# Performance work log

Measured on AMD Instinct MI355X. Metric: run time of the kernel, lower is better.

The kernel has to match this reference:

```python
import jax, jax.numpy as jnp
import numpy as np

PAD = -999
BATCH, NCHAIN, SEQ, NALT, NRES = 8, 2, 1024, 3, 20
NATOMS = 2_000_000
NATNAMES = 40
BACKBONE = jnp.array([0, 1, 2, 3], dtype=jnp.int32)  # N, CA, C, O atom-name ids
GLY = 7  # residue id treated as glycine (rsaSC forced to 0)
NBINS = BATCH * NCHAIN * SEQ * NALT


def setup_inputs() -> dict:
    key = jax.random.key(0)
    k = jax.random.split(key, 8)
    contRat = jax.random.uniform(k[0], (NATOMS, NALT), dtype=jnp.float32)
    atname = jax.random.randint(k[1], (NATOMS,), 0, NATNAMES, dtype=jnp.int32)
    # assign each atom to a (batch, chain, resnum) residue consistently
    resid = jax.random.randint(k[2], (NATOMS,), 0, BATCH * NCHAIN * SEQ, dtype=jnp.int32)
    batch = resid // (NCHAIN * SEQ)
    chain = (resid // SEQ) % NCHAIN
    resnum = resid % SEQ
    # residue type is a function of the residue (consistent across its atoms)
    resname_per_res = jax.random.randint(k[3], (BATCH * NCHAIN * SEQ,), 0, NRES, dtype=jnp.int32)
    resname = resname_per_res[resid]
    atom_description = jnp.stack([atname, resnum, chain, batch, resname], axis=1)
    alternatives = jax.random.bernoulli(k[4], 0.7, (NATOMS, NALT))
    # per-residue-type affine normalization points (max, min), max > min
    resMC_min = jax.random.uniform(k[5], (NRES,), dtype=jnp.float32) * 2.0
    resMC_max = resMC_min + 10.0 + jax.random.uniform(k[6], (NRES,), dtype=jnp.float32) * 20.0
    resSC_min = jax.random.uniform(k[7], (NRES,), dtype=jnp.float32) * 2.0
    resSC_max = resSC_min + 10.0 + jax.random.uniform(jax.random.fold_in(key, 99), (NRES,), dtype=jnp.float32) * 20.0
    return {
        "contRat": contRat,
        "resMC_max": resMC_max,
        "resMC_min": resMC_min,
        "resSC_max": resSC_max,
        "resSC_min": resSC_min,
        "atom_description": atom_description,
        "alternatives": alternatives,
    }


def _bind(contRat, resMC_max, resMC_min, resSC_max, resSC_min, atom_description, alternatives):
    atname = atom_description[:, 0]
    resnum = atom_description[:, 1]
    chain = atom_description[:, 2]
    batchInd = atom_description[:, 3]
    resname = atom_description[:, 4]

    is_backbone = jnp.isin(atname, BACKBONE)
    valid = atname != PAD

    # flat (batch, chain, resnum, alt) bin per atom per alternative
    base = (batchInd * NCHAIN + chain) * SEQ + resnum            # [natoms]
    flat = base[:, None] * NALT + jnp.arange(NALT, dtype=jnp.int32)[None, :]  # [natoms, nalt]

    maskMC = alternatives & (is_backbone & valid)[:, None]
    maskSC = alternatives & (~is_backbone & valid)[:, None]

    zero_idx = jnp.where(maskMC, flat, 0)
    rsaMC = jnp.zeros((NBINS,), contRat.dtype).at[zero_idx].add(
        jnp.where(maskMC, contRat, 0.0))
    rsaSC = jnp.zeros((NBINS,), contRat.dtype).at[jnp.where(maskSC, flat, 0)].add(
        jnp.where(maskSC, contRat, 0.0))

    # sequence: non-accumulating scatter of resname on the backbone path; dump
    # masked-out writes to an extra trailing bin
    seq_flat = jnp.full((NBINS + 1,), PAD, dtype=jnp.int32).at[
        jnp.where(maskMC, flat, NBINS)
    ].set(jnp.where(maskMC, resname[:, None], PAD))[:NBINS]

    shape = (BATCH, NCHAIN, SEQ, NALT)
    rsaMC = rsaMC.reshape(shape)
    rsaSC = rsaSC.reshape(shape)
    seq = seq_flat.reshape(shape)

    # per-residue-type affine normalization: (x - min) / (max - min)
    idx = jnp.clip(seq, 0, NRES - 1)
    has_res = seq != PAD
    rsaMC = jnp.where(has_res, (rsaMC - resMC_min[idx]) / (resMC_max[idx] - resMC_min[idx]), rsaMC)
    sc_norm = (rsaSC - resSC_min[idx]) / (resSC_max[idx] - resSC_min[idx])
    rsaSC = jnp.where(has_res & (seq != GLY), sc_norm,
                      jnp.where(has_res & (seq == GLY), 0.0, rsaSC))

    return jnp.clip(rsaMC, 0.0, 1.0), jnp.clip(rsaSC, 0.0, 1.0)


def reference(contRat, resMC_max, resMC_min, resSC_max, resSC_min, atom_description, alternatives):
    return _bind(contRat, resMC_max, resMC_min, resSC_max, resSC_min,
                 atom_description, alternatives)
```

## Files before the change

### kernel.cpp

```cpp
#include <hip/hip_runtime.h>


#define PADV   (-999)
#define BATCH  8
#define NCHAIN 2
#define SEQL   1024
#define NALT   3
#define NRES   20
#define NATOMS 2000000
#define GLY    7
#define NRESID (BATCH * NCHAIN * SEQL)
#define NBINS  (NRESID * NALT)
#define NCHUNK 8
#define CHSZ   (NRESID / NCHUNK)
#define SMAXSL 64

#define PK_R(w)    ((int)((w) & 16383u))
#define PK_BB(w)   (((w) >> 19) & 1u)
#define PK_AM(w)   ((w) >> 20)

__global__ __launch_bounds__(256)
void k_pack(const int* __restrict__ desc,
            const unsigned char* __restrict__ altB,
            const int* __restrict__ altI,
            unsigned* __restrict__ pack,
            int* __restrict__ seq) {
    const unsigned char probe = altB[(threadIdx.x & 63) * 4 + 1];
    const bool byteLayout = (__ballot(probe != 0) != 0ULL);

    const int t  = blockIdx.x * blockDim.x + threadIdx.x;
    const int a0 = t * 4;
    if (a0 >= NATOMS) return;

    const int4* d4 = (const int4*)(desc + (size_t)a0 * 5);
    int4 q0 = d4[0], q1 = d4[1], q2 = d4[2], q3 = d4[3], q4 = d4[4];
    int an[4], rn[4], ch[4], bi[4], rs[4];
    an[0]=q0.x; rn[0]=q0.y; ch[0]=q0.z; bi[0]=q0.w; rs[0]=q1.x;
    an[1]=q1.y; rn[1]=q1.z; ch[1]=q1.w; bi[1]=q2.x; rs[1]=q2.y;
    an[2]=q2.z; rn[2]=q2.w; ch[2]=q3.x; bi[2]=q3.y; rs[2]=q3.z;
    an[3]=q3.w; rn[3]=q4.x; ch[3]=q4.y; bi[3]=q4.z; rs[3]=q4.w;

    unsigned am[4];
    if (byteLayout) {
        const unsigned* b3 = (const unsigned*)(altB + (size_t)a0 * 3);
        unsigned w0 = b3[0], w1 = b3[1], w2 = b3[2];
        unsigned char f[12];
        f[0]=w0; f[1]=w0>>8; f[2]=w0>>16; f[3]=w0>>24;
        f[4]=w1; f[5]=w1>>8; f[6]=w1>>16; f[7]=w1>>24;
        f[8]=w2; f[9]=w2>>8; f[10]=w2>>16; f[11]=w2>>24;
        #pragma unroll
        for (int k = 0; k < 4; ++k)
            am[k] = (f[k*3+0]?1u:0u) | (f[k*3+1]?2u:0u) | (f[k*3+2]?4u:0u);
    } else {
        const int4* i4 = (const int4*)(altI + (size_t)a0 * 3);
        int4 w0 = i4[0], w1 = i4[1], w2 = i4[2];
        int f[12] = {w0.x,w0.y,w0.z,w0.w, w1.x,w1.y,w1.z,w1.w,
                     w2.x,w2.y,w2.z,w2.w};
        #pragma unroll
        for (int k = 0; k < 4; ++k)
            am[k] = (f[k*3+0]?1u:0u) | (f[k*3+1]?2u:0u) | (f[k*3+2]?4u:0u);
    }

    uint4 pw;
    unsigned* pwp = (unsigned*)&pw;
    #pragma unroll
    for (int k = 0; k < 4; ++k) {
        const bool valid = (an[k] != PADV);
        const bool bb    = ((unsigned)an[k] <= 3u);
        const int  r     = (bi[k] * NCHAIN + ch[k]) * SEQL + rn[k];
        const bool rOK   = ((unsigned)r < (unsigned)NRESID);
        const unsigned a = (valid && rOK) ? am[k] : 0u;
        const unsigned res = (unsigned)(rs[k] & 31);
        pwp[k] = (rOK ? (unsigned)r : 0u) | (res << 14)
               | ((bb ? 1u : 0u) << 19) | (a << 20);
        if (bb && a) {
            if (a & 1) seq[r * 3 + 0] = rs[k] & 31;
            if (a & 2) seq[r * 3 + 1] = rs[k] & 31;
            if (a & 4) seq[r * 3 + 2] = rs[k] & 31;
        }
    }
    *(uint4*)(pack + a0) = pw;
}

__global__ __launch_bounds__(1024)
void k_scan(const float* __restrict__ contRat,
            const unsigned* __restrict__ pack,
            float* __restrict__ part,
            int S, int sliceSz) {
    __shared__ float acc[6 * CHSZ];

    const int c = blockIdx.x & (NCHUNK - 1);
    const int s = blockIdx.x >> 3;

    for (int j = threadIdx.x; j < 6 * CHSZ; j += blockDim.x) acc[j] = 0.0f;
    __syncthreads();

    const int start = s * sliceSz;
    int end = start + sliceSz;
    if (end > NATOMS) end = NATOMS;

    int i = start + (int)threadIdx.x * 4;
    const int step = (int)blockDim.x * 4;

    #define PROCESS(w, idx)                                                   \
        do {                                                                  \
            const unsigned am_ = PK_AM(w);                                    \
            if (am_) {                                                        \
                const int r_ = PK_R(w);                                       \
                if ((r_ >> 11) == c) {                                        \
                    const int lr_ = r_ & (CHSZ - 1);                          \
                    const int pb_ = (PK_BB(w) ? 0 : 3) * CHSZ + lr_;          \
                    const float* cr_ = contRat + (size_t)(idx) * 3;           \
                    if (am_ & 1) atomicAdd(&acc[pb_ + 0 * CHSZ], cr_[0]);     \
                    if (am_ & 2) atomicAdd(&acc[pb_ + 1 * CHSZ], cr_[1]);     \
                    if (am_ & 4) atomicAdd(&acc[pb_ + 2 * CHSZ], cr_[2]);     \
                }                                                             \
            }                                                                 \
        } while (0)

    for (; i + 3 < end; i += step) {
        const uint4 w4 = *(const uint4*)(pack + i);
        PROCESS(w4.x, i);
        PROCESS(w4.y, i + 1);
        PROCESS(w4.z, i + 2);
        PROCESS(w4.w, i + 3);
    }
    for (int k = i; k < end && k < i + 4; ++k) PROCESS(pack[k], k);
    #undef PROCESS

    __syncthreads();

    for (int t = threadIdx.x; t < 6 * CHSZ; t += blockDim.x) {
        const int plane = t >> 11;
        const int j     = t & (CHSZ - 1);
        part[((size_t)s * 6 + plane) * NRESID + c * CHSZ + j] = acc[t];
    }
}

__global__ void k_reduce(const float* __restrict__ part, int S,
                         const int* __restrict__ seq,
                         float* __restrict__ out,
                         const float* __restrict__ mcmax,
                         const float* __restrict__ mcmin,
                         const float* __restrict__ scmax,
                         const float* __restrict__ scmin) {
    int t = blockIdx.x * blockDim.x + threadIdx.x;
    if (t >= NBINS) return;
    const int r   = t & (NRESID - 1);
    const int alt = t >> 14;

    float m = 0.0f, v = 0.0f;
    for (int s2 = 0; s2 < S; ++s2) {
        m += part[((size_t)s2 * 6 + alt) * NRESID + r];
        v += part[((size_t)s2 * 6 + 3 + alt) * NRESID + r];
    }

    const int f  = r * NALT + alt;
    const int sq = seq[f];
    if (sq >= 0) {
        int idx = (sq > NRES - 1) ? (NRES - 1) : sq;
        m = (m - mcmin[idx]) / (mcmax[idx] - mcmin[idx]);
        if (sq != GLY) v = (v - scmin[idx]) / (scmax[idx] - scmin[idx]);
        else           v = 0.0f;
    }
    out[f]         = fminf(fmaxf(m, 0.0f), 1.0f);
    out[NBINS + f] = fminf(fmaxf(v, 0.0f), 1.0f);
}

__global__ void k_init_flat(float* __restrict__ out, int* __restrict__ seq,
                            int* __restrict__ flag,
                            const unsigned char* __restrict__ altBytes) {
    int i = blockIdx.x * blockDim.x + threadIdx.x;
    if (i < NBINS) { out[i] = 0.0f; out[NBINS + i] = 0.0f; seq[i] = PADV; }
    if (blockIdx.x == 0 && threadIdx.x < 64) {
        unsigned char b = altBytes[threadIdx.x * 4 + 1];
        unsigned long long m = __ballot(b != 0);
        if (threadIdx.x == 0) *flag = (m != 0ULL) ? 1 : 0;
    }
}

__global__ void k_scatter_flat(const float* __restrict__ contRat,
                               const int* __restrict__ desc,
                               const unsigned char* __restrict__ altB,
                               const int* __restrict__ altI,
                               const int* __restrict__ flag,
                               float* __restrict__ mcArr,
                               float* __restrict__ scArr,
                               int* __restrict__ seq) {
    int a = blockIdx.x * blockDim.x + threadIdx.x;
    if (a >= NATOMS) return;
    const int atname  = desc[a * 5 + 0];
    const int resnum  = desc[a * 5 + 1];
    const int chain   = desc[a * 5 + 2];
    const int batchI  = desc[a * 5 + 3];
    const int resname = desc[a * 5 + 4];
    const bool valid = (atname != PADV);
    const bool is_bb = (atname >= 0) && (atname <= 3);
    const int  base  = ((batchI * NCHAIN + chain) * SEQL + resnum) * NALT;
    const bool byteLayout = (*flag != 0);
    #pragma unroll
    for (int alt = 0; alt < NALT; ++alt) {
        bool altv;
        if (byteLayout) altv = (altB[a * NALT + alt] != 0);
        else            altv = (altI[a * NALT + alt] != 0);
        if (altv && valid) {
            const float c = contRat[a * NALT + alt];
            const int   f = base + alt;
            if (is_bb) { atomicAdd(&mcArr[f], c); seq[f] = resname; }
            else       { atomicAdd(&scArr[f], c); }
        }
    }
}

__global__ void k_final_flat(float* __restrict__ mc, float* __restrict__ sc,
                             const int* __restrict__ seq,
                             const float* __restrict__ mcmax,
                             const float* __restrict__ mcmin,
                             const float* __restrict__ scmax,
                             const float* __restrict__ scmin) {
    int i = blockIdx.x * blockDim.x + threadIdx.x;
    if (i >= NBINS) return;
    const int s = seq[i];
    float m = mc[i], v = sc[i];
    if (s != PADV) {
        int idx = s < 0 ? 0 : (s > NRES - 1 ? NRES - 1 : s);
        m = (m - mcmin[idx]) / (mcmax[idx] - mcmin[idx]);
        if (s != GLY) v = (v - scmin[idx]) / (scmax[idx] - scmin[idx]);
        else          v = 0.0f;
    }
    mc[i] = fminf(fmaxf(m, 0.0f), 1.0f);
    sc[i] = fminf(fmaxf(v, 0.0f), 1.0f);
}

extern "C" void kernel_launch(void* const* d_in, const int* in_sizes, int n_in,
                              void* d_out, int out_size, void* d_ws, size_t ws_size,
                              hipStream_t stream) {
    const float* contRat = (const float*)d_in[0];
    const float* mcmax   = (const float*)d_in[1];
    const float* mcmin   = (const float*)d_in[2];
    const float* scmax   = (const float*)d_in[3];
    const float* scmin   = (const float*)d_in[4];
    const int*   desc    = (const int*)d_in[5];
    const void*  alts    = d_in[6];

    float* out = (float*)d_out;

    const size_t packBytes  = (size_t)NATOMS * sizeof(unsigned);
    const size_t seqBytes   = (size_t)NBINS * sizeof(int);
    const size_t sliceBytes = (size_t)6 * NRESID * sizeof(float);

    int S = 0;
    if (ws_size > packBytes + seqBytes + 64) {
        size_t s = (ws_size - packBytes - seqBytes - 64) / sliceBytes;
        S = (s > SMAXSL) ? SMAXSL : (int)s;
    }

    const int binBlocks = (NBINS + 255) / 256;

    if (S >= 2) {
        unsigned* pack = (unsigned*)d_ws;
        float*    part = (float*)((char*)d_ws + packBytes);
        int*      seq  = (int*)((char*)d_ws + packBytes + (size_t)S * sliceBytes);

        int sliceSz = (NATOMS + S - 1) / S;
        sliceSz = (sliceSz + 3) & ~3;

        k_pack<<<(NATOMS / 4 + 255) / 256, 256, 0, stream>>>(
            desc, (const unsigned char*)alts, (const int*)alts, pack, seq);
        k_scan<<<NCHUNK * S, 1024, 0, stream>>>(contRat, pack, part, S, sliceSz);
        k_reduce<<<binBlocks, 256, 0, stream>>>(
            part, S, seq, out, mcmax, mcmin, scmax, scmin);
    } else {
        int* seq  = (int*)d_ws;
        int* flag = seq + NBINS;
        k_init_flat<<<binBlocks, 256, 0, stream>>>(out, seq, flag,
                                                   (const unsigned char*)alts);
        k_scatter_flat<<<(NATOMS + 255) / 256, 256, 0, stream>>>(
            contRat, desc,
            (const unsigned char*)alts, (const int*)alts, flag,
            out, out + NBINS, seq);
        k_final_flat<<<binBlocks, 256, 0, stream>>>(
            out, out + NBINS, seq, mcmax, mcmin, scmax, scmin);
    }
}
```

Baseline: 181.7 us.

## Derive residue sequence via shared-memory atomicOr in scan, drop global seq scatter

Removes the scattered global writes of residue names from the pack kernel. The scan kernel now ORs a per-residue byte (backbone alt mask plus residue type) into shared memory and writes it as a per-slice partial, which the reduce kernel ORs across slices. The reduce is restructured to one thread per residue that handles all three alternatives, and the block-to-(chunk, slice) mapping now makes adjacent blocks share a chunk. This adds an extra shared atomic per backbone atom and relies on the residue type being consistent within a residue, and S is now rounded to a multiple of 8.

```diff
diff --git a/kernel.cpp b/kernel.cpp
--- a/kernel.cpp
+++ b/kernel.cpp
@@ -16,6 +16,7 @@
 #define SMAXSL 64
 
 #define PK_R(w)    ((int)((w) & 16383u))
+#define PK_RES(w)  (((w) >> 14) & 31u)
 #define PK_BB(w)   (((w) >> 19) & 1u)
 #define PK_AM(w)   ((w) >> 20)
 
@@ -23,8 +24,7 @@
 void k_pack(const int* __restrict__ desc,
             const unsigned char* __restrict__ altB,
             const int* __restrict__ altI,
-            unsigned* __restrict__ pack,
-            int* __restrict__ seq) {
+            unsigned* __restrict__ pack) {
     const unsigned char probe = altB[(threadIdx.x & 63) * 4 + 1];
     const bool byteLayout = (__ballot(probe != 0) != 0ULL);
 
@@ -70,14 +70,8 @@
         const int  r     = (bi[k] * NCHAIN + ch[k]) * SEQL + rn[k];
         const bool rOK   = ((unsigned)r < (unsigned)NRESID);
         const unsigned a = (valid && rOK) ? am[k] : 0u;
-        const unsigned res = (unsigned)(rs[k] & 31);
-        pwp[k] = (rOK ? (unsigned)r : 0u) | (res << 14)
+        pwp[k] = (rOK ? (unsigned)r : 0u) | ((unsigned)(rs[k] & 31) << 14)
                | ((bb ? 1u : 0u) << 19) | (a << 20);
-        if (bb && a) {
-            if (a & 1) seq[r * 3 + 0] = rs[k] & 31;
-            if (a & 2) seq[r * 3 + 1] = rs[k] & 31;
-            if (a & 4) seq[r * 3 + 2] = rs[k] & 31;
-        }
     }
     *(uint4*)(pack + a0) = pw;
 }
@@ -86,13 +80,16 @@
 void k_scan(const float* __restrict__ contRat,
             const unsigned* __restrict__ pack,
             float* __restrict__ part,
+            unsigned char* __restrict__ partRes,
             int S, int sliceSz) {
     __shared__ float acc[6 * CHSZ];
-
-    const int c = blockIdx.x & (NCHUNK - 1);
-    const int s = blockIdx.x >> 3;
+    __shared__ unsigned resOr[CHSZ];
+
+    const int c = blockIdx.x / S;
+    const int s = blockIdx.x - c * S;
 
     for (int j = threadIdx.x; j < 6 * CHSZ; j += blockDim.x) acc[j] = 0.0f;
+    for (int j = threadIdx.x; j < CHSZ; j += blockDim.x) resOr[j] = 0u;
     __syncthreads();
 
     const int start = s * sliceSz;
@@ -109,11 +106,17 @@
                 const int r_ = PK_R(w);                                       \
                 if ((r_ >> 11) == c) {                                        \
                     const int lr_ = r_ & (CHSZ - 1);                          \
-                    const int pb_ = (PK_BB(w) ? 0 : 3) * CHSZ + lr_;          \
                     const float* cr_ = contRat + (size_t)(idx) * 3;           \
-                    if (am_ & 1) atomicAdd(&acc[pb_ + 0 * CHSZ], cr_[0]);     \
-                    if (am_ & 2) atomicAdd(&acc[pb_ + 1 * CHSZ], cr_[1]);     \
-                    if (am_ & 4) atomicAdd(&acc[pb_ + 2 * CHSZ], cr_[2]);     \
+                    if (PK_BB(w)) {                                           \
+                        atomicOr(&resOr[lr_], (am_ << 5) | PK_RES(w));        \
+                        if (am_ & 1) atomicAdd(&acc[0 * CHSZ + lr_], cr_[0]); \
+                        if (am_ & 2) atomicAdd(&acc[1 * CHSZ + lr_], cr_[1]); \
+                        if (am_ & 4) atomicAdd(&acc[2 * CHSZ + lr_], cr_[2]); \
+                    } else {                                                  \
+                        if (am_ & 1) atomicAdd(&acc[3 * CHSZ + lr_], cr_[0]); \
+                        if (am_ & 2) atomicAdd(&acc[4 * CHSZ + lr_], cr_[1]); \
+                        if (am_ & 4) atomicAdd(&acc[5 * CHSZ + lr_], cr_[2]); \
+                    }                                                         \
                 }                                                             \
             }                                                                 \
         } while (0)
@@ -135,36 +138,48 @@
         const int j     = t & (CHSZ - 1);
         part[((size_t)s * 6 + plane) * NRESID + c * CHSZ + j] = acc[t];
     }
-}
-
-__global__ void k_reduce(const float* __restrict__ part, int S,
-                         const int* __restrict__ seq,
-                         float* __restrict__ out,
-                         const float* __restrict__ mcmax,
-                         const float* __restrict__ mcmin,
-                         const float* __restrict__ scmax,
-                         const float* __restrict__ scmin) {
-    int t = blockIdx.x * blockDim.x + threadIdx.x;
-    if (t >= NBINS) return;
-    const int r   = t & (NRESID - 1);
-    const int alt = t >> 14;
-
-    float m = 0.0f, v = 0.0f;
-    for (int s2 = 0; s2 < S; ++s2) {
-        m += part[((size_t)s2 * 6 + alt) * NRESID + r];
-        v += part[((size_t)s2 * 6 + 3 + alt) * NRESID + r];
-    }
-
-    const int f  = r * NALT + alt;
-    const int sq = seq[f];
-    if (sq >= 0) {
-        int idx = (sq > NRES - 1) ? (NRES - 1) : sq;
-        m = (m - mcmin[idx]) / (mcmax[idx] - mcmin[idx]);
-        if (sq != GLY) v = (v - scmin[idx]) / (scmax[idx] - scmin[idx]);
-        else           v = 0.0f;
-    }
-    out[f]         = fminf(fmaxf(m, 0.0f), 1.0f);
-    out[NBINS + f] = fminf(fmaxf(v, 0.0f), 1.0f);
+    for (int j = threadIdx.x; j < CHSZ; j += blockDim.x)
+        partRes[(size_t)s * NRESID + c * CHSZ + j] = (unsigned char)resOr[j];
+}
+
+__global__ __launch_bounds__(256)
+void k_reduce(const float* __restrict__ part,
+              const unsigned char* __restrict__ partRes, int S,
+              float* __restrict__ out,
+              const float* __restrict__ mcmax,
+              const float* __restrict__ mcmin,
+              const float* __restrict__ scmax,
+              const float* __restrict__ scmin) {
+    const int r = blockIdx.x * blockDim.x + threadIdx.x;
+    if (r >= NRESID) return;
+
+    float m0 = 0.f, m1 = 0.f, m2 = 0.f, v0 = 0.f, v1 = 0.f, v2 = 0.f;
+    unsigned rb = 0;
+    for (int s = 0; s < S; ++s) {
+        const float* b = part + (size_t)s * 6 * NRESID + r;
+        m0 += b[0 * NRESID]; m1 += b[1 * NRESID]; m2 += b[2 * NRESID];
+        v0 += b[3 * NRESID]; v1 += b[4 * NRESID]; v2 += b[5 * NRESID];
+        rb |= partRes[(size_t)s * NRESID + r];
+    }
+
+    const unsigned am = rb >> 5;
+    int resn = (int)(rb & 31u);
+    if (resn > NRES - 1) resn = NRES - 1;
+    const float mLo = mcmin[resn], mSpan = mcmax[resn] - mLo;
+    const float sLo = scmin[resn], sSpan = scmax[resn] - sLo;
+    const bool  gly = ((rb & 31u) == GLY);
+
+    float mv[3] = {m0, m1, m2}, vv[3] = {v0, v1, v2};
+    #pragma unroll
+    for (int alt = 0; alt < 3; ++alt) {
+        float m = mv[alt], v = vv[alt];
+        if ((am >> alt) & 1u) {
+            m = (m - mLo) / mSpan;
+            v = gly ? 0.0f : (v - sLo) / sSpan;
+        }
+        out[r * 3 + alt]         = fminf(fmaxf(m, 0.0f), 1.0f);
+        out[NBINS + r * 3 + alt] = fminf(fmaxf(v, 0.0f), 1.0f);
+    }
 }
 
 __global__ void k_init_flat(float* __restrict__ out, int* __restrict__ seq,
@@ -246,33 +261,35 @@
     float* out = (float*)d_out;
 
     const size_t packBytes  = (size_t)NATOMS * sizeof(unsigned);
-    const size_t seqBytes   = (size_t)NBINS * sizeof(int);
-    const size_t sliceBytes = (size_t)6 * NRESID * sizeof(float);
+    const size_t sliceBytes = (size_t)6 * NRESID * sizeof(float)
+                            + (size_t)NRESID;
 
     int S = 0;
-    if (ws_size > packBytes + seqBytes + 64) {
-        size_t s = (ws_size - packBytes - seqBytes - 64) / sliceBytes;
+    if (ws_size > packBytes + 64) {
+        size_t s = (ws_size - packBytes - 64) / sliceBytes;
         S = (s > SMAXSL) ? SMAXSL : (int)s;
-    }
-
-    const int binBlocks = (NBINS + 255) / 256;
-
-    if (S >= 2) {
-        unsigned* pack = (unsigned*)d_ws;
-        float*    part = (float*)((char*)d_ws + packBytes);
-        int*      seq  = (int*)((char*)d_ws + packBytes + (size_t)S * sliceBytes);
+        S &= ~7;
+    }
+
+    if (S >= 8) {
+        unsigned*      pack    = (unsigned*)d_ws;
+        float*         part    = (float*)((char*)d_ws + packBytes);
+        unsigned char* partRes = (unsigned char*)((char*)d_ws + packBytes +
+                                 (size_t)S * 6 * NRESID * sizeof(float));
 
         int sliceSz = (NATOMS + S - 1) / S;
         sliceSz = (sliceSz + 3) & ~3;
 
         k_pack<<<(NATOMS / 4 + 255) / 256, 256, 0, stream>>>(
-            desc, (const unsigned char*)alts, (const int*)alts, pack, seq);
-        k_scan<<<NCHUNK * S, 1024, 0, stream>>>(contRat, pack, part, S, sliceSz);
-        k_reduce<<<binBlocks, 256, 0, stream>>>(
-            part, S, seq, out, mcmax, mcmin, scmax, scmin);
+            desc, (const unsigned char*)alts, (const int*)alts, pack);
+        k_scan<<<NCHUNK * S, 1024, 0, stream>>>(
+            contRat, pack, part, partRes, S, sliceSz);
+        k_reduce<<<(NRESID + 255) / 256, 256, 0, stream>>>(
+            part, partRes, S, out, mcmax, mcmin, scmax, scmin);
     } else {
         int* seq  = (int*)d_ws;
         int* flag = seq + NBINS;
+        const int binBlocks = (NBINS + 255) / 256;
         k_init_flat<<<binBlocks, 256, 0, stream>>>(out, seq, flag,
                                                    (const unsigned char*)alts);
         k_scatter_flat<<<(NATOMS + 255) / 256, 256, 0, stream>>>(
```

New measurement: 188.7 us. 3.9% more time.

## Replace sliced shared-memory scan with counting-sort by residue bucket then accumulate

Applied to the files above, without the earlier changes.

Replaces the pack + chunked-scan + partial-reduce pipeline with a counting sort. Atoms are bucketed by residue group (256 buckets of 64 residues) using per-block histograms, a two-level prefix scan and a scatter into a sorted index array. Each bucket is then accumulated in small shared-memory tiles split across 8 sub-blocks, and the residue name for seq is derived via atomicOr instead of a separate scatter. This avoids every scan block re-reading the whole pack array and removes the large partial-sum reduction. In exchange it adds six launches, a global scatter of 8-byte entries with random contRat gathers, and a larger workspace requirement.

```diff
diff --git a/kernel.cpp b/kernel.cpp
--- a/kernel.cpp
+++ b/kernel.cpp
@@ -11,160 +11,245 @@
 #define GLY    7
 #define NRESID (BATCH * NCHAIN * SEQL)
 #define NBINS  (NRESID * NALT)
-#define NCHUNK 8
-#define CHSZ   (NRESID / NCHUNK)
-#define SMAXSL 64
+#define NBLK   ((NATOMS + 1023) / 1024)
+#define NBUCK  256
+#define ACC_SUB 8
 
 #define PK_R(w)    ((int)((w) & 16383u))
+#define PK_RES(w)  (((w) >> 14) & 31u)
 #define PK_BB(w)   (((w) >> 19) & 1u)
 #define PK_AM(w)   ((w) >> 20)
 
-__global__ __launch_bounds__(256)
-void k_pack(const int* __restrict__ desc,
-            const unsigned char* __restrict__ altB,
-            const int* __restrict__ altI,
-            unsigned* __restrict__ pack,
-            int* __restrict__ seq) {
+#define OFF_PACK  ((size_t)0)
+#define SZ_PACK   ((size_t)NATOMS * 4)
+#define OFF_HIST  (OFF_PACK + SZ_PACK)
+#define SZ_HIST   ((size_t)NBUCK * NBLK * 4)
+#define OFF_BB    (OFF_HIST + SZ_HIST)
+#define SZ_BB     ((size_t)1280)
+#define OFF_TOT   (OFF_BB + SZ_BB)
+#define SZ_TOT    ((size_t)1024)
+#define OFF_SORT  (OFF_TOT + SZ_TOT)
+#define SZ_SORT   ((size_t)NATOMS * 8)
+#define OFF_ACC   (OFF_SORT + SZ_SORT)
+#define SZ_ACC    ((size_t)NBUCK * ACC_SUB * 384 * 4)
+#define OFF_RES   (OFF_ACC + SZ_ACC)
+#define SZ_RES    ((size_t)NBUCK * ACC_SUB * 64 * 4)
+#define WS_NEED   (OFF_RES + SZ_RES)
+
+__global__ __launch_bounds__(256)
+void k_pack_hist(const int* __restrict__ desc,
+                 const unsigned char* __restrict__ altB,
+                 const int* __restrict__ altI,
+                 unsigned* __restrict__ pack,
+                 unsigned* __restrict__ hist) {
+    __shared__ unsigned h[NBUCK];
+    for (int j = threadIdx.x; j < NBUCK; j += 256) h[j] = 0u;
+    __syncthreads();
+
     const unsigned char probe = altB[(threadIdx.x & 63) * 4 + 1];
     const bool byteLayout = (__ballot(probe != 0) != 0ULL);
 
-    const int t  = blockIdx.x * blockDim.x + threadIdx.x;
-    const int a0 = t * 4;
-    if (a0 >= NATOMS) return;
-
-    const int4* d4 = (const int4*)(desc + (size_t)a0 * 5);
-    int4 q0 = d4[0], q1 = d4[1], q2 = d4[2], q3 = d4[3], q4 = d4[4];
-    int an[4], rn[4], ch[4], bi[4], rs[4];
-    an[0]=q0.x; rn[0]=q0.y; ch[0]=q0.z; bi[0]=q0.w; rs[0]=q1.x;
-    an[1]=q1.y; rn[1]=q1.z; ch[1]=q1.w; bi[1]=q2.x; rs[1]=q2.y;
-    an[2]=q2.z; rn[2]=q2.w; ch[2]=q3.x; bi[2]=q3.y; rs[2]=q3.z;
-    an[3]=q3.w; rn[3]=q4.x; ch[3]=q4.y; bi[3]=q4.z; rs[3]=q4.w;
-
-    unsigned am[4];
-    if (byteLayout) {
-        const unsigned* b3 = (const unsigned*)(altB + (size_t)a0 * 3);
-        unsigned w0 = b3[0], w1 = b3[1], w2 = b3[2];
-        unsigned char f[12];
-        f[0]=w0; f[1]=w0>>8; f[2]=w0>>16; f[3]=w0>>24;
-        f[4]=w1; f[5]=w1>>8; f[6]=w1>>16; f[7]=w1>>24;
-        f[8]=w2; f[9]=w2>>8; f[10]=w2>>16; f[11]=w2>>24;
+    const int a0 = (blockIdx.x * 256 + threadIdx.x) * 4;
+    if (a0 < NATOMS) {
+        const int4* d4 = (const int4*)(desc + (size_t)a0 * 5);
+        int4 q0 = d4[0], q1 = d4[1], q2 = d4[2], q3 = d4[3], q4 = d4[4];
+        int an[4], rn[4], ch[4], bi[4], rs[4];
+        an[0]=q0.x; rn[0]=q0.y; ch[0]=q0.z; bi[0]=q0.w; rs[0]=q1.x;
+        an[1]=q1.y; rn[1]=q1.z; ch[1]=q1.w; bi[1]=q2.x; rs[1]=q2.y;
+        an[2]=q2.z; rn[2]=q2.w; ch[2]=q3.x; bi[2]=q3.y; rs[2]=q3.z;
+        an[3]=q3.w; rn[3]=q4.x; ch[3]=q4.y; bi[3]=q4.z; rs[3]=q4.w;
+
+        unsigned am[4];
+        if (byteLayout) {
+            const unsigned* b3 = (const unsigned*)(altB + (size_t)a0 * 3);
+            unsigned w0 = b3[0], w1 = b3[1], w2 = b3[2];
+            unsigned char f[12];
+            f[0]=w0; f[1]=w0>>8; f[2]=w0>>16; f[3]=w0>>24;
+            f[4]=w1; f[5]=w1>>8; f[6]=w1>>16; f[7]=w1>>24;
+            f[8]=w2; f[9]=w2>>8; f[10]=w2>>16; f[11]=w2>>24;
+            #pragma unroll
+            for (int k = 0; k < 4; ++k)
+                am[k] = (f[k*3+0]?1u:0u) | (f[k*3+1]?2u:0u) | (f[k*3+2]?4u:0u);
+        } else {
+            const int4* i4 = (const int4*)(altI + (size_t)a0 * 3);
+            int4 w0 = i4[0], w1 = i4[1], w2 = i4[2];
+            int f[12] = {w0.x,w0.y,w0.z,w0.w, w1.x,w1.y,w1.z,w1.w,
+                         w2.x,w2.y,w2.z,w2.w};
+            #pragma unroll
+            for (int k = 0; k < 4; ++k)
+                am[k] = (f[k*3+0]?1u:0u) | (f[k*3+1]?2u:0u) | (f[k*3+2]?4u:0u);
+        }
+
+        uint4 pw;
+        unsigned* pwp = (unsigned*)&pw;
         #pragma unroll
-        for (int k = 0; k < 4; ++k)
-            am[k] = (f[k*3+0]?1u:0u) | (f[k*3+1]?2u:0u) | (f[k*3+2]?4u:0u);
-    } else {
-        const int4* i4 = (const int4*)(altI + (size_t)a0 * 3);
-        int4 w0 = i4[0], w1 = i4[1], w2 = i4[2];
-        int f[12] = {w0.x,w0.y,w0.z,w0.w, w1.x,w1.y,w1.z,w1.w,
-                     w2.x,w2.y,w2.z,w2.w};
+        for (int k = 0; k < 4; ++k) {
+            const bool valid = (an[k] != PADV);
+            const bool bb    = ((unsigned)an[k] <= 3u);
+            const int  r     = (bi[k] * NCHAIN + ch[k]) * SEQL + rn[k];
+            const bool rOK   = ((unsigned)r < (unsigned)NRESID);
+            const unsigned a = (valid && rOK) ? am[k] : 0u;
+            pwp[k] = (rOK ? (unsigned)r : 0u)
+                   | ((unsigned)(rs[k] & 31) << 14)
+                   | ((bb ? 1u : 0u) << 19) | (a << 20);
+            if (a) atomicAdd(&h[(pwp[k] >> 6) & 255u], 1u);
+        }
+        *(uint4*)(pack + a0) = pw;
+    }
+    __syncthreads();
+    for (int j = threadIdx.x; j < NBUCK; j += 256)
+        hist[(size_t)j * NBLK + blockIdx.x] = h[j];
+}
+
+__global__ __launch_bounds__(256)
+void k_prefix1(unsigned* __restrict__ hist, unsigned* __restrict__ totals) {
+    __shared__ unsigned cnt[2048];
+    __shared__ unsigned csum[256];
+    unsigned* h = hist + (size_t)blockIdx.x * NBLK;
+    const int t = threadIdx.x;
+
+    for (int j = t; j < 2048; j += 256) cnt[j] = (j < NBLK) ? h[j] : 0u;
+    __syncthreads();
+
+    unsigned s = 0;
+    #pragma unroll
+    for (int k = 0; k < 8; ++k) s += cnt[t * 8 + k];
+    csum[t] = s;
+    __syncthreads();
+    for (int off = 1; off < 256; off <<= 1) {
+        unsigned x = (t >= off) ? csum[t - off] : 0u;
+        __syncthreads();
+        csum[t] += x;
+        __syncthreads();
+    }
+    if (t == 255) totals[blockIdx.x] = csum[255];
+    unsigned run = (t == 0) ? 0u : csum[t - 1];
+    #pragma unroll
+    for (int k = 0; k < 8; ++k) {
+        const int idx = t * 8 + k;
+        const unsigned old = cnt[idx];
+        cnt[idx] = run;
+        run += old;
+    }
+    __syncthreads();
+    for (int j = t; j < NBLK; j += 256) h[j] = cnt[j];
+}
+
+__global__ __launch_bounds__(256)
+void k_prefix2(const unsigned* __restrict__ totals,
+               unsigned* __restrict__ bucketBase) {
+    __shared__ unsigned s[256];
+    const int t = threadIdx.x;
+    const unsigned own = totals[t];
+    s[t] = own;
+    __syncthreads();
+    for (int off = 1; off < 256; off <<= 1) {
+        unsigned x = (t >= off) ? s[t - off] : 0u;
+        __syncthreads();
+        s[t] += x;
+        __syncthreads();
+    }
+    bucketBase[t] = s[t] - own;
+    if (t == 255) bucketBase[256] = s[255];
+}
+
+__global__ __launch_bounds__(256)
+void k_scatter(const unsigned* __restrict__ pack,
+               const unsigned* __restrict__ hist,
+               const unsigned* __restrict__ bucketBase,
+               uint2* __restrict__ sorted) {
+    __shared__ unsigned lbase[NBUCK];
+    for (int j = threadIdx.x; j < NBUCK; j += 256)
+        lbase[j] = bucketBase[j] + hist[(size_t)j * NBLK + blockIdx.x];
+    __syncthreads();
+
+    const int a0 = (blockIdx.x * 256 + threadIdx.x) * 4;
+    if (a0 < NATOMS) {
+        const uint4 pw = *(const uint4*)(pack + a0);
+        const unsigned* pwp = (const unsigned*)&pw;
         #pragma unroll
-        for (int k = 0; k < 4; ++k)
-            am[k] = (f[k*3+0]?1u:0u) | (f[k*3+1]?2u:0u) | (f[k*3+2]?4u:0u);
-    }
-
-    uint4 pw;
-    unsigned* pwp = (unsigned*)&pw;
+        for (int k = 0; k < 4; ++k) {
+            const unsigned w = pwp[k];
+            if (w >> 20) {
+                const unsigned b   = (w >> 6) & 255u;
+                const unsigned pos = atomicAdd(&lbase[b], 1u);
+                sorted[pos] = make_uint2(w, (unsigned)(a0 + k));
+            }
+        }
+    }
+}
+
+__global__ __launch_bounds__(256)
+void k_accum(const uint2* __restrict__ sorted,
+             const float* __restrict__ contRat,
+             const unsigned* __restrict__ bucketBase,
+             float* __restrict__ accPart,
+             unsigned* __restrict__ resPart) {
+    __shared__ float acc[6 * 64];
+    __shared__ unsigned ror[64];
+    const int b   = blockIdx.x >> 3;
+    const int sub = blockIdx.x & 7;
+
+    for (int j = threadIdx.x; j < 384; j += 256) acc[j] = 0.0f;
+    if (threadIdx.x < 64) ror[threadIdx.x] = 0u;
+    __syncthreads();
+
+    const unsigned s0 = bucketBase[b], s1 = bucketBase[b + 1];
+    const unsigned len = s1 - s0;
+    const unsigned lo = s0 + (unsigned)(((unsigned long long)len * sub) >> 3);
+    const unsigned hi = s0 + (unsigned)(((unsigned long long)len * (sub + 1)) >> 3);
+
+    for (unsigned i = lo + threadIdx.x; i < hi; i += 256) {
+        const uint2 e = sorted[i];
+        const unsigned w = e.x;
+        const int lr = (int)(w & 63u);
+        const unsigned am = PK_AM(w);
+        const float* cr = contRat + (size_t)e.y * 3;
+        const int pb = PK_BB(w) ? 0 : 3;
+        if (PK_BB(w)) atomicOr(&ror[lr], (am << 5) | PK_RES(w));
+        if (am & 1) atomicAdd(&acc[(pb + 0) * 64 + lr], cr[0]);
+        if (am & 2) atomicAdd(&acc[(pb + 1) * 64 + lr], cr[1]);
+        if (am & 4) atomicAdd(&acc[(pb + 2) * 64 + lr], cr[2]);
+    }
+    __syncthreads();
+
+    float* ap = accPart + ((size_t)b * ACC_SUB + sub) * 384;
+    for (int j = threadIdx.x; j < 384; j += 256) ap[j] = acc[j];
+    if (threadIdx.x < 64)
+        resPart[((size_t)b * ACC_SUB + sub) * 64 + threadIdx.x] = ror[threadIdx.x];
+}
+
+__global__ __launch_bounds__(192)
+void k_finalize(const float* __restrict__ accPart,
+                const unsigned* __restrict__ resPart,
+                float* __restrict__ out,
+                const float* __restrict__ mcmax,
+                const float* __restrict__ mcmin,
+                const float* __restrict__ scmax,
+                const float* __restrict__ scmin) {
+    const int b = blockIdx.x;
+    const int t = threadIdx.x;
+    const int lr = t / 3, alt = t - lr * 3;
+
+    float m = 0.0f, v = 0.0f;
+    unsigned rb = 0u;
     #pragma unroll
-    for (int k = 0; k < 4; ++k) {
-        const bool valid = (an[k] != PADV);
-        const bool bb    = ((unsigned)an[k] <= 3u);
-        const int  r     = (bi[k] * NCHAIN + ch[k]) * SEQL + rn[k];
-        const bool rOK   = ((unsigned)r < (unsigned)NRESID);
-        const unsigned a = (valid && rOK) ? am[k] : 0u;
-        const unsigned res = (unsigned)(rs[k] & 31);
-        pwp[k] = (rOK ? (unsigned)r : 0u) | (res << 14)
-               | ((bb ? 1u : 0u) << 19) | (a << 20);
-        if (bb && a) {
-            if (a & 1) seq[r * 3 + 0] = rs[k] & 31;
-            if (a & 2) seq[r * 3 + 1] = rs[k] & 31;
-            if (a & 4) seq[r * 3 + 2] = rs[k] & 31;
-        }
-    }
-    *(uint4*)(pack + a0) = pw;
-}
-
-__global__ __launch_bounds__(1024)
-void k_scan(const float* __restrict__ contRat,
-            const unsigned* __restrict__ pack,
-            float* __restrict__ part,
-            int S, int sliceSz) {
-    __shared__ float acc[6 * CHSZ];
-
-    const int c = blockIdx.x & (NCHUNK - 1);
-    const int s = blockIdx.x >> 3;
-
-    for (int j = threadIdx.x; j < 6 * CHSZ; j += blockDim.x) acc[j] = 0.0f;
-    __syncthreads();
-
-    const int start = s * sliceSz;
-    int end = start + sliceSz;
-    if (end > NATOMS) end = NATOMS;
-
-    int i = start + (int)threadIdx.x * 4;
-    const int step = (int)blockDim.x * 4;
-
-    #define PROCESS(w, idx)                                                   \
-        do {                                                                  \
-            const unsigned am_ = PK_AM(w);                                    \
-            if (am_) {                                                        \
-                const int r_ = PK_R(w);                                       \
-                if ((r_ >> 11) == c) {                                        \
-                    const int lr_ = r_ & (CHSZ - 1);                          \
-                    const int pb_ = (PK_BB(w) ? 0 : 3) * CHSZ + lr_;          \
-                    const float* cr_ = contRat + (size_t)(idx) * 3;           \
-                    if (am_ & 1) atomicAdd(&acc[pb_ + 0 * CHSZ], cr_[0]);     \
-                    if (am_ & 2) atomicAdd(&acc[pb_ + 1 * CHSZ], cr_[1]);     \
-                    if (am_ & 4) atomicAdd(&acc[pb_ + 2 * CHSZ], cr_[2]);     \
-                }                                                             \
-            }                                                                 \
-        } while (0)
-
-    for (; i + 3 < end; i += step) {
-        const uint4 w4 = *(const uint4*)(pack + i);
-        PROCESS(w4.x, i);
-        PROCESS(w4.y, i + 1);
-        PROCESS(w4.z, i + 2);
-        PROCESS(w4.w, i + 3);
-    }
-    for (int k = i; k < end && k < i + 4; ++k) PROCESS(pack[k], k);
-    #undef PROCESS
-
-    __syncthreads();
-
-    for (int t = threadIdx.x; t < 6 * CHSZ; t += blockDim.x) {
-        const int plane = t >> 11;
-        const int j     = t & (CHSZ - 1);
-        part[((size_t)s * 6 + plane) * NRESID + c * CHSZ + j] = acc[t];
-    }
-}
-
-__global__ void k_reduce(const float* __restrict__ part, int S,
-                         const int* __restrict__ seq,
-                         float* __restrict__ out,
-                         const float* __restrict__ mcmax,
-                         const float* __restrict__ mcmin,
-                         const float* __restrict__ scmax,
-                         const float* __restrict__ scmin) {
-    int t = blockIdx.x * blockDim.x + threadIdx.x;
-    if (t >= NBINS) return;
-    const int r   = t & (NRESID - 1);
-    const int alt = t >> 14;
-
-    float m = 0.0f, v = 0.0f;
-    for (int s2 = 0; s2 < S; ++s2) {
-        m += part[((size_t)s2 * 6 + alt) * NRESID + r];
-        v += part[((size_t)s2 * 6 + 3 + alt) * NRESID + r];
-    }
-
-    const int f  = r * NALT + alt;
-    const int sq = seq[f];
-    if (sq >= 0) {
-        int idx = (sq > NRES - 1) ? (NRES - 1) : sq;
-        m = (m - mcmin[idx]) / (mcmax[idx] - mcmin[idx]);
-        if (sq != GLY) v = (v - scmin[idx]) / (scmax[idx] - scmin[idx]);
-        else           v = 0.0f;
-    }
-    out[f]         = fminf(fmaxf(m, 0.0f), 1.0f);
-    out[NBINS + f] = fminf(fmaxf(v, 0.0f), 1.0f);
+    for (int s = 0; s < ACC_SUB; ++s) {
+        const float* ap = accPart + ((size_t)b * ACC_SUB + s) * 384;
+        m  += ap[alt * 64 + lr];
+        v  += ap[(3 + alt) * 64 + lr];
+        rb |= resPart[((size_t)b * ACC_SUB + s) * 64 + lr];
+    }
+
+    if ((rb >> (5 + alt)) & 1u) {
+        int resn = (int)(rb & 31u);
+        if (resn > NRES - 1) resn = NRES - 1;
+        m = (m - mcmin[resn]) / (mcmax[resn] - mcmin[resn]);
+        v = ((rb & 31u) == GLY) ? 0.0f
+                                : (v - scmin[resn]) / (scmax[resn] - scmin[resn]);
+    }
+    out[b * 192 + t]         = fminf(fmaxf(m, 0.0f), 1.0f);
+    out[NBINS + b * 192 + t] = fminf(fmaxf(v, 0.0f), 1.0f);
 }
 
 __global__ void k_init_flat(float* __restrict__ out, int* __restrict__ seq,
@@ -245,34 +330,28 @@
 
     float* out = (float*)d_out;
 
-    const size_t packBytes  = (size_t)NATOMS * sizeof(unsigned);
-    const size_t seqBytes   = (size_t)NBINS * sizeof(int);
-    const size_t sliceBytes = (size_t)6 * NRESID * sizeof(float);
-
-    int S = 0;
-    if (ws_size > packBytes + seqBytes + 64) {
-        size_t s = (ws_size - packBytes - seqBytes - 64) / sliceBytes;
-        S = (s > SMAXSL) ? SMAXSL : (int)s;
-    }
-
-    const int binBlocks = (NBINS + 255) / 256;
-
-    if (S >= 2) {
-        unsigned* pack = (unsigned*)d_ws;
-        float*    part = (float*)((char*)d_ws + packBytes);
-        int*      seq  = (int*)((char*)d_ws + packBytes + (size_t)S * sliceBytes);
-
-        int sliceSz = (NATOMS + S - 1) / S;
-        sliceSz = (sliceSz + 3) & ~3;
-
-        k_pack<<<(NATOMS / 4 + 255) / 256, 256, 0, stream>>>(
-            desc, (const unsigned char*)alts, (const int*)alts, pack, seq);
-        k_scan<<<NCHUNK * S, 1024, 0, stream>>>(contRat, pack, part, S, sliceSz);
-        k_reduce<<<binBlocks, 256, 0, stream>>>(
-            part, S, seq, out, mcmax, mcmin, scmax, scmin);
+    if (ws_size >= WS_NEED) {
+        unsigned* pack  = (unsigned*)((char*)d_ws + OFF_PACK);
+        unsigned* hist  = (unsigned*)((char*)d_ws + OFF_HIST);
+        unsigned* bbase = (unsigned*)((char*)d_ws + OFF_BB);
+        unsigned* tot   = (unsigned*)((char*)d_ws + OFF_TOT);
+        uint2*    sorted= (uint2*)   ((char*)d_ws + OFF_SORT);
+        float*    accP  = (float*)   ((char*)d_ws + OFF_ACC);
+        unsigned* resP  = (unsigned*)((char*)d_ws + OFF_RES);
+
+        k_pack_hist<<<NBLK, 256, 0, stream>>>(
+            desc, (const unsigned char*)alts, (const int*)alts, pack, hist);
+        k_prefix1<<<NBUCK, 256, 0, stream>>>(hist, tot);
+        k_prefix2<<<1, 256, 0, stream>>>(tot, bbase);
+        k_scatter<<<NBLK, 256, 0, stream>>>(pack, hist, bbase, sorted);
+        k_accum<<<NBUCK * ACC_SUB, 256, 0, stream>>>(
+            sorted, contRat, bbase, accP, resP);
+        k_finalize<<<NBUCK, 192, 0, stream>>>(
+            accP, resP, out, mcmax, mcmin, scmax, scmin);
     } else {
         int* seq  = (int*)d_ws;
         int* flag = seq + NBINS;
+        const int binBlocks = (NBINS + 255) / 256;
         k_init_flat<<<binBlocks, 256, 0, stream>>>(out, seq, flag,
                                                    (const unsigned char*)alts);
         k_scatter_flat<<<(NATOMS + 255) / 256, 256, 0, stream>>>(
```

After: 170.1 us. 1.07x faster.
